# Kernel tuning notes

Hardware: AMD Instinct MI355X
Metric: run time of the kernel (lower is better)

## Reference

```python
import jax, jax.numpy as jnp
import numpy as np

N_NODES = 100000
N_EDGES = 625000
D_IN = 128
D_OUT = 128


def setup_inputs() -> dict:
    key = jax.random.key(0)
    k1, k2, k3, k4, k5 = jax.random.split(key, 5)
    scale = 1.0 / np.sqrt(D_IN)
    x = jax.random.normal(k1, (N_NODES, D_IN), dtype=jnp.float32)
    edge_index = jax.random.randint(k2, (2, N_EDGES), 0, N_NODES, dtype=jnp.int64)
    W_l = jax.random.normal(k3, (D_IN, D_OUT), dtype=jnp.float32) * scale
    b_l = jax.random.normal(k4, (D_OUT,), dtype=jnp.float32) * scale
    W_r = jax.random.normal(k5, (D_IN, D_OUT), dtype=jnp.float32) * scale
    return {"x": x, "edge_index": edge_index, "W_l": W_l, "b_l": b_l, "W_r": W_r}


def reference(x, edge_index, W_l, b_l, W_r):
    # SAGEConv (mean aggr, no self loops):
    #   out = lin_l(mean_{j in N(i)} x_j) + lin_r(x_i)
    src = edge_index[0]  # message source nodes
    dst = edge_index[1]  # aggregation targets
    n = x.shape[0]
    msgs = x[src]  # [E, D_IN] gather
    agg = jax.ops.segment_sum(msgs, dst, num_segments=n)  # [N, D_IN]
    deg = jax.ops.segment_sum(jnp.ones_like(dst, dtype=x.dtype), dst, num_segments=n)
    mean = agg / jnp.maximum(deg, 1.0)[:, None]  # isolated nodes -> 0
    return mean @ W_l + b_l + x @ W_r
```

## Files before the change

### kernel.cpp

```cpp
#include <hip/hip_runtime.h>


constexpr int N_NODES = 100000;
constexpr int N_EDGES = 625000;
constexpr int D = 128;
constexpr int SCAN_CHUNK = 1024;
constexpr int N_SCAN_BLOCKS = (N_NODES + SCAN_CHUNK - 1) / SCAN_CHUNK;
constexpr int CONV_BLOCKS = N_NODES * D / (512 * 4);
constexpr int ZERO_BLOCKS = (N_NODES / 4 + 255) / 256;
constexpr int E4 = N_EDGES / 4;

typedef __attribute__((ext_vector_type(8))) short short8;
typedef __attribute__((ext_vector_type(4))) short short4v;
typedef __attribute__((ext_vector_type(4))) float f32x4;

__device__ __forceinline__ unsigned short f2bf(float f) {
    union { float f; unsigned int u; } c; c.f = f;
    unsigned int u = c.u + 0x7fffu + ((c.u >> 16) & 1u);
    return (unsigned short)(u >> 16);
}
__device__ __forceinline__ float bflo(unsigned int v) {
    union { unsigned int u; float f; } c; c.u = v << 16; return c.f;
}
__device__ __forceinline__ float bfhi(unsigned int v) {
    union { unsigned int u; float f; } c; c.u = v & 0xffff0000u; return c.f;
}
__device__ __forceinline__ uint2 pack4(float4 a) {
    uint2 r;
    r.x = (unsigned)f2bf(a.x) | ((unsigned)f2bf(a.y) << 16);
    r.y = (unsigned)f2bf(a.z) | ((unsigned)f2bf(a.w) << 16);
    return r;
}

__global__ __launch_bounds__(256) void conv_all(
    const float* __restrict__ x, const float* __restrict__ Wl,
    const float* __restrict__ Wr,
    unsigned short* __restrict__ xb, unsigned short* __restrict__ wT,
    int* __restrict__ cnt)
{
    const int tid = threadIdx.x;
    if (blockIdx.x < CONV_BLOCKS) {
        __shared__ uint2 ls[512];
        const float4* xp = (const float4*)x;
        const int base = blockIdx.x * 512;
        float4 v0 = xp[base + tid];
        float4 v1 = xp[base + 256 + tid];
        ls[tid]       = pack4(v0);
        ls[tid + 256] = pack4(v1);
        __syncthreads();
        uint4 q = ((const uint4*)ls)[tid];
        ((uint4*)xb)[base / 2 + tid] = q;
    } else if (blockIdx.x < CONV_BLOCKS + 16) {
        int flat = (blockIdx.x - CONV_BLOCKS) * 256 + tid;
        int k  = flat >> 4;
        int n0 = (flat & 15) * 8;
        const float* Wsrc = (k < 128) ? &Wl[k * 128 + n0] : &Wr[(k - 128) * 128 + n0];
        float4 a = *(const float4*)Wsrc;
        float4 b = *(const float4*)(Wsrc + 4);
        wT[(n0 + 0) * 256 + k] = f2bf(a.x);
        wT[(n0 + 1) * 256 + k] = f2bf(a.y);
        wT[(n0 + 2) * 256 + k] = f2bf(a.z);
        wT[(n0 + 3) * 256 + k] = f2bf(a.w);
        wT[(n0 + 4) * 256 + k] = f2bf(b.x);
        wT[(n0 + 5) * 256 + k] = f2bf(b.y);
        wT[(n0 + 6) * 256 + k] = f2bf(b.z);
        wT[(n0 + 7) * 256 + k] = f2bf(b.w);
    } else {
        int t3 = (blockIdx.x - CONV_BLOCKS - 16) * 256 + tid;
        if (t3 < N_NODES / 4) ((uint4*)cnt)[t3] = make_uint4(0, 0, 0, 0);
    }
}

__global__ __launch_bounds__(256) void hist4(
    const int* __restrict__ dst, int* __restrict__ cnt)
{
    int t = blockIdx.x * 256 + threadIdx.x;
    if (t < E4) {
        int e = t * 4;
        int4 d4 = *(const int4*)&dst[e];
        atomicAdd(&cnt[d4.x], 1);
        atomicAdd(&cnt[d4.y], 1);
        atomicAdd(&cnt[d4.z], 1);
        atomicAdd(&cnt[d4.w], 1);
    }
}

__global__ __launch_bounds__(256) void scan_blocks(
    const int* __restrict__ cnt, int* __restrict__ ptr, int* __restrict__ bsums)
{
    __shared__ int sh[256];
    const int t = threadIdx.x;
    const int base = blockIdx.x * SCAN_CHUNK + t * 4;
    int v0 = (base + 0 < N_NODES) ? cnt[base + 0] : 0;
    int v1 = (base + 1 < N_NODES) ? cnt[base + 1] : 0;
    int v2 = (base + 2 < N_NODES) ? cnt[base + 2] : 0;
    int v3 = (base + 3 < N_NODES) ? cnt[base + 3] : 0;
    const int tsum = v0 + v1 + v2 + v3;
    sh[t] = tsum;
    __syncthreads();
    #pragma unroll
    for (int off = 1; off < 256; off <<= 1) {
        int val = (t >= off) ? sh[t - off] : 0;
        __syncthreads();
        sh[t] += val;
        __syncthreads();
    }
    const int texcl = sh[t] - tsum;
    if (t == 255) bsums[blockIdx.x] = sh[255];
    int e0 = texcl, e1 = e0 + v0, e2 = e1 + v1, e3 = e2 + v2;
    if (base + 0 < N_NODES) ptr[base + 0] = e0;
    if (base + 1 < N_NODES) ptr[base + 1] = e1;
    if (base + 2 < N_NODES) ptr[base + 2] = e2;
    if (base + 3 < N_NODES) ptr[base + 3] = e3;
}

__global__ __launch_bounds__(256) void add_offsets_fused(
    int* __restrict__ ptr, int* __restrict__ cursor, const int* __restrict__ bsums)
{
    __shared__ int sh[256];
    const int t = threadIdx.x;
    int v = (t < blockIdx.x) ? bsums[t] : 0;
    sh[t] = v;
    __syncthreads();
    #pragma unroll
    for (int off = 128; off > 0; off >>= 1) {
        if (t < off) sh[t] += sh[t + off];
        __syncthreads();
    }
    const int soff = sh[0];
    const int base = blockIdx.x * SCAN_CHUNK + t * 4;
    #pragma unroll
    for (int j = 0; j < 4; ++j) {
        int i = base + j;
        if (i < N_NODES) {
            int p = ptr[i] + soff;
            ptr[i] = p;
            cursor[i] = p;
        }
    }
    if (blockIdx.x == 0 && t == 0) ptr[N_NODES] = N_EDGES;
}

__global__ __launch_bounds__(256) void csr_fill(
    const int* __restrict__ src, const int* __restrict__ dst,
    int* __restrict__ cursor, int* __restrict__ sorted_src)
{
    int t = blockIdx.x * 256 + threadIdx.x;
    if (t < E4) {
        int e = t * 4;
        int4 d4 = *(const int4*)&dst[e];
        int4 s4 = *(const int4*)&src[e];
        int p0 = atomicAdd(&cursor[d4.x], 1);
        int p1 = atomicAdd(&cursor[d4.y], 1);
        int p2 = atomicAdd(&cursor[d4.z], 1);
        int p3 = atomicAdd(&cursor[d4.w], 1);
        sorted_src[p0] = s4.x;
        sorted_src[p1] = s4.y;
        sorted_src[p2] = s4.z;
        sorted_src[p3] = s4.w;
    }
}

__global__ __launch_bounds__(256) void sage_fused(
    const unsigned short* __restrict__ xb,
    const int* __restrict__ ptr,
    const int* __restrict__ sorted_src,
    const unsigned short* __restrict__ wT,
    const float* __restrict__ bl,
    float* __restrict__ out)
{
    __shared__ unsigned short sA[32 * 256];

    const int tid  = threadIdx.x;
    const int lane = tid & 63;
    const int w    = tid >> 6;
    const int l15  = lane & 15;
    const int lg   = lane >> 4;

    const int n0 = w * 32 + l15;
    const int n1 = n0 + 16;

    short8 B0[8], B1[8];
    #pragma unroll
    for (int s = 0; s < 8; ++s) {
        B0[s] = *(const short8*)&wT[(size_t)n0 * 256 + s * 32 + lg * 8];
        B1[s] = *(const short8*)&wT[(size_t)n1 * 256 + s * 32 + lg * 8];
    }
    const float bias0 = bl[n0];
    const float bias1 = bl[n1];

    const int row0 = blockIdx.x * 32;

    #pragma unroll
    for (int i = 0; i < 2; ++i) {
        int c = tid + i * 256;
        int r = c >> 4;
        int s = 16 + (c & 15);
        short8 v = *(const short8*)&xb[(size_t)(row0 + r) * D + (c & 15) * 8];
        *(short8*)&sA[r * 256 + ((s ^ (r & 7)) << 3)] = v;
    }

    {
        const int g = tid >> 4;
        const int l = tid & 15;
        const size_t off = (size_t)l * 8;

        auto gather_row = [&](int r) {
            const int node = row0 + r;
            const int beg = ptr[node];
            const int end = ptr[node + 1];
            float a0=0,a1=0,a2=0,a3=0,a4=0,a5=0,a6=0,a7=0;
            float b0=0,b1=0,b2=0,b3=0,b4=0,b5=0,b6=0,b7=0;
            float c0=0,c1=0,c2=0,c3=0,c4=0,c5=0,c6=0,c7=0;
            float d0=0,d1=0,d2=0,d3=0,d4=0,d5=0,d6=0,d7=0;
            for (int i = beg; i < end; i += 4) {
                int last = end - 1;
                int e1 = i + 1 < end ? i + 1 : last;
                int e2 = i + 2 < end ? i + 2 : last;
                int e3 = i + 3 < end ? i + 3 : last;
                float w1 = (i + 1 < end) ? 1.f : 0.f;
                float w2 = (i + 2 < end) ? 1.f : 0.f;
                float w3 = (i + 3 < end) ? 1.f : 0.f;
                int s0 = sorted_src[i],  s1 = sorted_src[e1];
                int s2 = sorted_src[e2], s3 = sorted_src[e3];
                uint4 v0 = *(const uint4*)&xb[(size_t)s0 * D + off];
                uint4 v1 = *(const uint4*)&xb[(size_t)s1 * D + off];
                uint4 v2 = *(const uint4*)&xb[(size_t)s2 * D + off];
                uint4 v3 = *(const uint4*)&xb[(size_t)s3 * D + off];
                a0+=bflo(v0.x); a1+=bfhi(v0.x); a2+=bflo(v0.y); a3+=bfhi(v0.y);
                a4+=bflo(v0.z); a5+=bfhi(v0.z); a6+=bflo(v0.w); a7+=bfhi(v0.w);
                b0=fmaf(w1,bflo(v1.x),b0); b1=fmaf(w1,bfhi(v1.x),b1);
                b2=fmaf(w1,bflo(v1.y),b2); b3=fmaf(w1,bfhi(v1.y),b3);
                b4=fmaf(w1,bflo(v1.z),b4); b5=fmaf(w1,bfhi(v1.z),b5);
                b6=fmaf(w1,bflo(v1.w),b6); b7=fmaf(w1,bfhi(v1.w),b7);
                c0=fmaf(w2,bflo(v2.x),c0); c1=fmaf(w2,bfhi(v2.x),c1);
                c2=fmaf(w2,bflo(v2.y),c2); c3=fmaf(w2,bfhi(v2.y),c3);
                c4=fmaf(w2,bflo(v2.z),c4); c5=fmaf(w2,bfhi(v2.z),c5);
                c6=fmaf(w2,bflo(v2.w),c6); c7=fmaf(w2,bfhi(v2.w),c7);
                d0=fmaf(w3,bflo(v3.x),d0); d1=fmaf(w3,bfhi(v3.x),d1);
                d2=fmaf(w3,bflo(v3.y),d2); d3=fmaf(w3,bfhi(v3.y),d3);
                d4=fmaf(w3,bflo(v3.z),d4); d5=fmaf(w3,bfhi(v3.z),d5);
                d6=fmaf(w3,bflo(v3.w),d6); d7=fmaf(w3,bfhi(v3.w),d7);
            }
            const float sc = 1.0f / fmaxf((float)(end - beg), 1.0f);
            uint4 o;
            o.x = (unsigned)f2bf(((a0+b0)+(c0+d0))*sc) | ((unsigned)f2bf(((a1+b1)+(c1+d1))*sc) << 16);
            o.y = (unsigned)f2bf(((a2+b2)+(c2+d2))*sc) | ((unsigned)f2bf(((a3+b3)+(c3+d3))*sc) << 16);
            o.z = (unsigned)f2bf(((a4+b4)+(c4+d4))*sc) | ((unsigned)f2bf(((a5+b5)+(c5+d5))*sc) << 16);
            o.w = (unsigned)f2bf(((a6+b6)+(c6+d6))*sc) | ((unsigned)f2bf(((a7+b7)+(c7+d7))*sc) << 16);
            *(uint4*)&sA[r * 256 + ((l ^ (r & 7)) << 3)] = o;
        };
        gather_row(g);
        gather_row(g + 16);
    }
    __syncthreads();

    const int a_r0 = l15;
    const int a_r1 = 16 + l15;

    f32x4 acc00 = {0.f,0.f,0.f,0.f}, acc01 = {0.f,0.f,0.f,0.f};
    f32x4 acc10 = {0.f,0.f,0.f,0.f}, acc11 = {0.f,0.f,0.f,0.f};

    #pragma unroll
    for (int s = 0; s < 8; ++s) {
        int ks = s * 4 + lg;
        short8 a0 = *(const short8*)&sA[a_r0 * 256 + ((ks ^ (a_r0 & 7)) << 3)];
        short8 a1 = *(const short8*)&sA[a_r1 * 256 + ((ks ^ (a_r1 & 7)) << 3)];
        acc00 = __builtin_amdgcn_mfma_f32_16x16x32_bf16(a0, B0[s], acc00, 0, 0, 0);
        acc01 = __builtin_amdgcn_mfma_f32_16x16x32_bf16(a0, B1[s], acc01, 0, 0, 0);
        acc10 = __builtin_amdgcn_mfma_f32_16x16x32_bf16(a1, B0[s], acc10, 0, 0, 0);
        acc11 = __builtin_amdgcn_mfma_f32_16x16x32_bf16(a1, B1[s], acc11, 0, 0, 0);
    }

    #pragma unroll
    for (int reg = 0; reg < 4; ++reg) {
        int r0w = row0 + lg * 4 + reg;
        int r1w = r0w + 16;
        out[(size_t)r0w * D + n0] = acc00[reg] + bias0;
        out[(size_t)r0w * D + n1] = acc01[reg] + bias1;
        out[(size_t)r1w * D + n0] = acc10[reg] + bias0;
        out[(size_t)r1w * D + n1] = acc11[reg] + bias1;
    }
}

__global__ __launch_bounds__(256) void wt_build(
    const float* __restrict__ Wl, const float* __restrict__ Wr,
    unsigned short* __restrict__ wT)
{
    int idx = blockIdx.x * 256 + threadIdx.x;
    if (idx >= 128 * 256) return;
    int n = idx >> 8;
    int k = idx & 255;
    float v = (k < 128) ? Wl[k * 128 + n] : Wr[(k - 128) * 128 + n];
    wT[n * 256 + k] = f2bf(v);
}

__global__ __launch_bounds__(256) void sage_aggregate(
    const float* __restrict__ x,
    const int* __restrict__ ptr,
    const int* __restrict__ sorted_src,
    float* __restrict__ mean)
{
    const int node = blockIdx.x * 4 + (threadIdx.x >> 6);
    if (node >= N_NODES) return;
    const int lane = threadIdx.x & 63;
    const int beg = ptr[node];
    const int end = ptr[node + 1];

    float2 acc0 = make_float2(0.f, 0.f);
    float2 acc1 = make_float2(0.f, 0.f);
    int i = beg;
    for (; i + 1 < end; i += 2) {
        int s0 = sorted_src[i];
        int s1 = sorted_src[i + 1];
        float2 a = *(const float2*)&x[(size_t)s0 * D + lane * 2];
        float2 b = *(const float2*)&x[(size_t)s1 * D + lane * 2];
        acc0.x += a.x; acc0.y += a.y;
        acc1.x += b.x; acc1.y += b.y;
    }
    if (i < end) {
        int s0 = sorted_src[i];
        float2 a = *(const float2*)&x[(size_t)s0 * D + lane * 2];
        acc0.x += a.x; acc0.y += a.y;
    }
    const float sc = 1.0f / fmaxf((float)(end - beg), 1.0f);
    float2 r = make_float2((acc0.x + acc1.x) * sc, (acc0.y + acc1.y) * sc);
    *(float2*)&mean[(size_t)node * D + lane * 2] = r;
}

__global__ __launch_bounds__(256) void sage_gemm_mfma(
    const float* __restrict__ x,
    const unsigned short* __restrict__ wT,
    const float* __restrict__ bl,
    float* __restrict__ out)
{
    __shared__ unsigned short sW[128 * 256];
    __shared__ unsigned short sA1[32 * 256];

    const int tid  = threadIdx.x;
    const int lane = tid & 63;
    const int w    = tid >> 6;
    const int l15  = lane & 15;
    const int lg   = lane >> 4;

    #pragma unroll
    for (int i = 0; i < 16; ++i) {
        int c  = tid + i * 256;
        int n  = c >> 5;
        int k8 = c & 31;
        short8 v = ((const short8*)wT)[c];
        *(short8*)&sW[n * 256 + ((k8 ^ (n & 7)) << 3)] = v;
    }

    const int a_r0 = l15;
    const int a_r1 = 16 + l15;
    const int n0 = w * 32 + l15;
    const int n1 = n0 + 16;
    const float bias0 = bl[n0];
    const float bias1 = bl[n1];
    const int nTiles = N_NODES / 32;

    for (int tile = blockIdx.x; tile < nTiles; tile += gridDim.x) {
        const int row0 = tile * 32;
        #pragma unroll
        for (int i = 0; i < 8; ++i) {
            int c    = tid + i * 256;
            int r    = c >> 6;
            int half = (c >> 5) & 1;
            int f4   = c & 31;
            const float* srcp = half ? &x[(size_t)(row0 + r) * D + f4 * 4]
                                     : &out[(size_t)(row0 + r) * D + f4 * 4];
            float4 v = *(const float4*)srcp;
            short4v b;
            b.x = (short)f2bf(v.x); b.y = (short)f2bf(v.y);
            b.z = (short)f2bf(v.z); b.w = (short)f2bf(v.w);
            int k = half * 128 + f4 * 4;
            int u = k >> 3;
            *(short4v*)&sA1[r * 256 + ((u ^ (r & 7)) << 3) + (k & 7)] = b;
        }
        __syncthreads();

        f32x4 acc00 = {0.f,0.f,0.f,0.f}, acc01 = {0.f,0.f,0.f,0.f};
        f32x4 acc10 = {0.f,0.f,0.f,0.f}, acc11 = {0.f,0.f,0.f,0.f};

        #pragma unroll
        for (int s = 0; s < 8; ++s) {
            int ks = s * 4 + lg;
            short8 a0 = *(const short8*)&sA1[a_r0 * 256 + ((ks ^ (a_r0 & 7)) << 3)];
            short8 a1 = *(const short8*)&sA1[a_r1 * 256 + ((ks ^ (a_r1 & 7)) << 3)];
            short8 b0 = *(const short8*)&sW[n0 * 256 + ((ks ^ (n0 & 7)) << 3)];
            short8 b1 = *(const short8*)&sW[n1 * 256 + ((ks ^ (n1 & 7)) << 3)];
            acc00 = __builtin_amdgcn_mfma_f32_16x16x32_bf16(a0, b0, acc00, 0, 0, 0);
            acc01 = __builtin_amdgcn_mfma_f32_16x16x32_bf16(a0, b1, acc01, 0, 0, 0);
            acc10 = __builtin_amdgcn_mfma_f32_16x16x32_bf16(a1, b0, acc10, 0, 0, 0);
            acc11 = __builtin_amdgcn_mfma_f32_16x16x32_bf16(a1, b1, acc11, 0, 0, 0);
        }
        __syncthreads();

        #pragma unroll
        for (int reg = 0; reg < 4; ++reg) {
            int r0w = row0 + lg * 4 + reg;
            int r1w = r0w + 16;
            out[(size_t)r0w * D + n0] = acc00[reg] + bias0;
            out[(size_t)r0w * D + n1] = acc01[reg] + bias1;
            out[(size_t)r1w * D + n0] = acc10[reg] + bias0;
            out[(size_t)r1w * D + n1] = acc11[reg] + bias1;
        }
    }
}

__global__ __launch_bounds__(256) void sage_scatter(
    const float* __restrict__ x, const int* __restrict__ src,
    const int* __restrict__ dst, float* __restrict__ agg, float* __restrict__ deg)
{
    int gid = blockIdx.x * 256 + threadIdx.x;
    int e = gid >> 7;
    if (e >= N_EDGES) return;
    int d = gid & 127;
    atomicAdd(&agg[(size_t)dst[e] * D + d], x[(size_t)src[e] * D + d]);
    if (d == 0) atomicAdd(&deg[dst[e]], 1.0f);
}

__global__ __launch_bounds__(256) void apply_mean(
    float* __restrict__ agg, const float* __restrict__ deg)
{
    int gid = blockIdx.x * 256 + threadIdx.x;
    int row = gid >> 5;
    if (row >= N_NODES) return;
    float sc = 1.0f / fmaxf(deg[row], 1.0f);
    float4 v = ((float4*)agg)[gid];
    v.x *= sc; v.y *= sc; v.z *= sc; v.w *= sc;
    ((float4*)agg)[gid] = v;
}

__device__ __forceinline__ void accum_tile(
    float acc[4][4], const float (*sWf)[D], const float (*srow)[D], int h, int j4)
{
    #pragma unroll 2
    for (int k = 0; k < D; k += 4) {
        float4 w0 = *(const float4*)&sWf[k + 0][j4];
        float4 w1 = *(const float4*)&sWf[k + 1][j4];
        float4 w2 = *(const float4*)&sWf[k + 2][j4];
        float4 w3 = *(const float4*)&sWf[k + 3][j4];
        #pragma unroll
        for (int r = 0; r < 4; ++r) {
            float4 a = *(const float4*)&srow[h + r * 8][k];
            acc[r][0] = fmaf(a.x, w0.x, fmaf(a.y, w1.x, fmaf(a.z, w2.x, fmaf(a.w, w3.x, acc[r][0]))));
            acc[r][1] = fmaf(a.x, w0.y, fmaf(a.y, w1.y, fmaf(a.z, w2.y, fmaf(a.w, w3.y, acc[r][1]))));
            acc[r][2] = fmaf(a.x, w0.z, fmaf(a.y, w1.z, fmaf(a.z, w2.z, fmaf(a.w, w3.z, acc[r][2]))));
            acc[r][3] = fmaf(a.x, w0.w, fmaf(a.y, w1.w, fmaf(a.z, w2.w, fmaf(a.w, w3.w, acc[r][3]))));
        }
    }
}

__global__ __launch_bounds__(256) void sage_gemm_f32(
    const float* __restrict__ x, const float* __restrict__ Wl,
    const float* __restrict__ bl, const float* __restrict__ Wr,
    float* __restrict__ out)
{
    __shared__ float sWf[D][D];
    __shared__ float srow[32][D];
    const int tid = threadIdx.x;
    const int j4 = (tid & 31) * 4;
    const int h  = tid >> 5;
    const int nTiles = (N_NODES + 31) / 32;
    const float4 bias = *(const float4*)(bl + j4);

    for (int tile = blockIdx.x; tile < nTiles; tile += gridDim.x) {
        const int row0 = tile * 32;
        float acc[4][4];
        #pragma unroll
        for (int r = 0; r < 4; ++r)
            #pragma unroll
            for (int c = 0; c < 4; ++c) acc[r][c] = 0.0f;

        __syncthreads();
        #pragma unroll
        for (int i = 0; i < 16; ++i)
            ((float4*)sWf)[tid + i * 256] = ((const float4*)Wl)[tid + i * 256];
        #pragma unroll
        for (int i = 0; i < 4; ++i) {
            int idx = tid + i * 256, r = idx >> 5, c = idx & 31, row = row0 + r;
            float4 v = make_float4(0.f,0.f,0.f,0.f);
            if (row < N_NODES) v = ((const float4*)out)[(size_t)row * 32 + c];
            ((float4*)srow)[idx] = v;
        }
        __syncthreads();
        accum_tile(acc, sWf, srow, h, j4);

        __syncthreads();
        #pragma unroll
        for (int i = 0; i < 16; ++i)
            ((float4*)sWf)[tid + i * 256] = ((const float4*)Wr)[tid + i * 256];
        #pragma unroll
        for (int i = 0; i < 4; ++i) {
            int idx = tid + i * 256, r = idx >> 5, c = idx & 31, row = row0 + r;
            float4 v = make_float4(0.f,0.f,0.f,0.f);
            if (row < N_NODES) v = ((const float4*)x)[(size_t)row * 32 + c];
            ((float4*)srow)[idx] = v;
        }
        __syncthreads();
        accum_tile(acc, sWf, srow, h, j4);

        #pragma unroll
        for (int r = 0; r < 4; ++r) {
            int row = row0 + h + r * 8;
            if (row < N_NODES) {
                float4 v = make_float4(acc[r][0] + bias.x, acc[r][1] + bias.y,
                                       acc[r][2] + bias.z, acc[r][3] + bias.w);
                *(float4*)(out + (size_t)row * D + j4) = v;
            }
        }
    }
}

extern "C" void kernel_launch(void* const* d_in, const int* in_sizes, int n_in,
                              void* d_out, int out_size, void* d_ws, size_t ws_size,
                              hipStream_t stream) {
    const float* x   = (const float*)d_in[0];
    const int*   ei  = (const int*)d_in[1];
    const float* Wl  = (const float*)d_in[2];
    const float* bl  = (const float*)d_in[3];
    const float* Wr  = (const float*)d_in[4];
    float* out = (float*)d_out;

    const int* src = ei;
    const int* dst = ei + N_EDGES;

    int* cnt    = (int*)d_ws;
    int* ptr    = cnt + N_NODES;
    int* cursor = ptr + N_NODES + 1;
    int* bsums  = cursor + N_NODES;
    int* sorted = bsums + 128;
    size_t int_count = (size_t)(3 * N_NODES + 1 + 128 + N_EDGES);
    int_count = (int_count + 7) & ~(size_t)7;
    unsigned short* wT = (unsigned short*)((int*)d_ws + int_count);
    unsigned short* xb = wT + 128 * 256;

    size_t need_B = int_count * sizeof(int);
    size_t need_A = need_B + 128 * 256 * 2 + (size_t)N_NODES * D * 2;

    if (ws_size >= need_A) {
        conv_all<<<CONV_BLOCKS + 16 + ZERO_BLOCKS, 256, 0, stream>>>(
            x, Wl, Wr, xb, wT, cnt);
        hist4<<<(E4 + 255) / 256, 256, 0, stream>>>(dst, cnt);
        scan_blocks<<<N_SCAN_BLOCKS, 256, 0, stream>>>(cnt, ptr, bsums);
        add_offsets_fused<<<N_SCAN_BLOCKS, 256, 0, stream>>>(ptr, cursor, bsums);
        csr_fill<<<(E4 + 255) / 256, 256, 0, stream>>>(src, dst, cursor, sorted);
        sage_fused<<<N_NODES / 32, 256, 0, stream>>>(xb, ptr, sorted, wT, bl, out);
    } else if (ws_size >= need_B) {
        hipMemsetAsync(cnt, 0, (size_t)N_NODES * sizeof(int), stream);
        hist4<<<(E4 + 255) / 256, 256, 0, stream>>>(dst, cnt);
        scan_blocks<<<N_SCAN_BLOCKS, 256, 0, stream>>>(cnt, ptr, bsums);
        add_offsets_fused<<<N_SCAN_BLOCKS, 256, 0, stream>>>(ptr, cursor, bsums);
        csr_fill<<<(E4 + 255) / 256, 256, 0, stream>>>(src, dst, cursor, sorted);
        unsigned short* wTc = (unsigned short*)cursor;
        wt_build<<<(128 * 256 + 255) / 256, 256, 0, stream>>>(Wl, Wr, wTc);
        sage_aggregate<<<(N_NODES + 3) / 4, 256, 0, stream>>>(x, ptr, sorted, out);
        sage_gemm_mfma<<<512, 256, 0, stream>>>(x, wTc, bl, out);
    } else {
        float* deg = (float*)d_ws;
        hipMemsetAsync(out, 0, (size_t)N_NODES * D * sizeof(float), stream);
        hipMemsetAsync(deg, 0, (size_t)N_NODES * sizeof(float), stream);
        long long total = (long long)N_EDGES * 128;
        sage_scatter<<<(int)((total + 255) / 256), 256, 0, stream>>>(x, src, dst, out, deg);
        apply_mean<<<(N_NODES * 32 + 255) / 256, 256, 0, stream>>>(out, deg);
        sage_gemm_f32<<<512, 256, 0, stream>>>(x, Wl, bl, Wr, out);
    }
}
```

Measured before the change: 139.5 us.

## Gather neighbor features from per-row int8-quantized copy instead of bf16

The conversion kernel now also writes an int8 copy of x with one absmax scale per row, alongside the bf16 copy. The fused SAGE kernel gathers neighbor rows from this int8 buffer, halving the bytes per random gather, and rescales each row by its scale during accumulation. Each thread now handles one node with 16 features instead of two nodes with 8, and the weight fragments load after the gather to lower register pressure during it. This adds quantization error to the mean aggregation, an extra write pass in the conversion kernel, and more dequantize ALU work.

```diff
diff --git a/kernel.cpp b/kernel.cpp
--- a/kernel.cpp
+++ b/kernel.cpp
@@ -6,7 +6,7 @@
 constexpr int D = 128;
 constexpr int SCAN_CHUNK = 1024;
 constexpr int N_SCAN_BLOCKS = (N_NODES + SCAN_CHUNK - 1) / SCAN_CHUNK;
-constexpr int CONV_BLOCKS = N_NODES * D / (512 * 4);
+constexpr int CONV2_BLOCKS = N_NODES / 16;
 constexpr int ZERO_BLOCKS = (N_NODES / 4 + 255) / 256;
 constexpr int E4 = N_EDGES / 4;
 
@@ -18,12 +18,6 @@
     union { float f; unsigned int u; } c; c.f = f;
     unsigned int u = c.u + 0x7fffu + ((c.u >> 16) & 1u);
     return (unsigned short)(u >> 16);
-}
-__device__ __forceinline__ float bflo(unsigned int v) {
-    union { unsigned int u; float f; } c; c.u = v << 16; return c.f;
-}
-__device__ __forceinline__ float bfhi(unsigned int v) {
-    union { unsigned int u; float f; } c; c.u = v & 0xffff0000u; return c.f;
 }
 __device__ __forceinline__ uint2 pack4(float4 a) {
     uint2 r;
@@ -31,27 +25,52 @@
     r.y = (unsigned)f2bf(a.z) | ((unsigned)f2bf(a.w) << 16);
     return r;
 }
+__device__ __forceinline__ void i8x4_to_f32(unsigned q, float* o) {
+    o[0] = (float)(int)(signed char)(q & 0xff);
+    o[1] = (float)(int)(signed char)((q >> 8) & 0xff);
+    o[2] = (float)(int)(signed char)((q >> 16) & 0xff);
+    o[3] = (float)(int)(signed char)(q >> 24);
+}
 
 __global__ __launch_bounds__(256) void conv_all(
     const float* __restrict__ x, const float* __restrict__ Wl,
     const float* __restrict__ Wr,
-    unsigned short* __restrict__ xb, unsigned short* __restrict__ wT,
-    int* __restrict__ cnt)
+    unsigned short* __restrict__ xb, unsigned char* __restrict__ x8,
+    float* __restrict__ scales,
+    unsigned short* __restrict__ wT, int* __restrict__ cnt)
 {
     const int tid = threadIdx.x;
-    if (blockIdx.x < CONV_BLOCKS) {
-        __shared__ uint2 ls[512];
+    if (blockIdx.x < CONV2_BLOCKS) {
+        const int g = tid >> 4;
+        const int l = tid & 15;
+        const int row = blockIdx.x * 16 + g;
         const float4* xp = (const float4*)x;
-        const int base = blockIdx.x * 512;
-        float4 v0 = xp[base + tid];
-        float4 v1 = xp[base + 256 + tid];
-        ls[tid]       = pack4(v0);
-        ls[tid + 256] = pack4(v1);
-        __syncthreads();
-        uint4 q = ((const uint4*)ls)[tid];
-        ((uint4*)xb)[base / 2 + tid] = q;
-    } else if (blockIdx.x < CONV_BLOCKS + 16) {
-        int flat = (blockIdx.x - CONV_BLOCKS) * 256 + tid;
+        const int f4a = row * 32 + l;
+        const int f4b = f4a + 16;
+        float4 v0 = xp[f4a];
+        float4 v1 = xp[f4b];
+        float m = fmaxf(fmaxf(fmaxf(fabsf(v0.x), fabsf(v0.y)), fmaxf(fabsf(v0.z), fabsf(v0.w))),
+                        fmaxf(fmaxf(fabsf(v1.x), fabsf(v1.y)), fmaxf(fabsf(v1.z), fabsf(v1.w))));
+        #pragma unroll
+        for (int off = 1; off < 16; off <<= 1)
+            m = fmaxf(m, __shfl_xor(m, off, 16));
+        const float s   = m * (1.0f / 127.0f);
+        const float inv = (m > 0.0f) ? 127.0f / m : 0.0f;
+        if (l == 0) scales[row] = s;
+        auto q4 = [&](float4 v) -> unsigned {
+            int a0 = (int)rintf(v.x * inv);
+            int a1 = (int)rintf(v.y * inv);
+            int a2 = (int)rintf(v.z * inv);
+            int a3 = (int)rintf(v.w * inv);
+            return (unsigned)(a0 & 0xff) | ((unsigned)(a1 & 0xff) << 8) |
+                   ((unsigned)(a2 & 0xff) << 16) | ((unsigned)(a3 & 0xff) << 24);
+        };
+        ((unsigned*)x8)[f4a] = q4(v0);
+        ((unsigned*)x8)[f4b] = q4(v1);
+        ((uint2*)xb)[f4a] = pack4(v0);
+        ((uint2*)xb)[f4b] = pack4(v1);
+    } else if (blockIdx.x < CONV2_BLOCKS + 16) {
+        int flat = (blockIdx.x - CONV2_BLOCKS) * 256 + tid;
         int k  = flat >> 4;
         int n0 = (flat & 15) * 8;
         const float* Wsrc = (k < 128) ? &Wl[k * 128 + n0] : &Wr[(k - 128) * 128 + n0];
@@ -66,7 +85,7 @@
         wT[(n0 + 6) * 256 + k] = f2bf(b.z);
         wT[(n0 + 7) * 256 + k] = f2bf(b.w);
     } else {
-        int t3 = (blockIdx.x - CONV_BLOCKS - 16) * 256 + tid;
+        int t3 = (blockIdx.x - CONV2_BLOCKS - 16) * 256 + tid;
         if (t3 < N_NODES / 4) ((uint4*)cnt)[t3] = make_uint4(0, 0, 0, 0);
     }
 }
@@ -163,6 +182,8 @@
 
 __global__ __launch_bounds__(256) void sage_fused(
     const unsigned short* __restrict__ xb,
+    const unsigned char* __restrict__ x8,
+    const float* __restrict__ scales,
     const int* __restrict__ ptr,
     const int* __restrict__ sorted_src,
     const unsigned short* __restrict__ wT,
@@ -176,18 +197,6 @@
     const int w    = tid >> 6;
     const int l15  = lane & 15;
     const int lg   = lane >> 4;
-
-    const int n0 = w * 32 + l15;
-    const int n1 = n0 + 16;
-
-    short8 B0[8], B1[8];
-    #pragma unroll
-    for (int s = 0; s < 8; ++s) {
-        B0[s] = *(const short8*)&wT[(size_t)n0 * 256 + s * 32 + lg * 8];
-        B1[s] = *(const short8*)&wT[(size_t)n1 * 256 + s * 32 + lg * 8];
-    }
-    const float bias0 = bl[n0];
-    const float bias1 = bl[n1];
 
     const int row0 = blockIdx.x * 32;
 
@@ -201,59 +210,92 @@
     }
 
     {
-        const int g = tid >> 4;
-        const int l = tid & 15;
-        const size_t off = (size_t)l * 8;
-
-        auto gather_row = [&](int r) {
-            const int node = row0 + r;
-            const int beg = ptr[node];
-            const int end = ptr[node + 1];
-            float a0=0,a1=0,a2=0,a3=0,a4=0,a5=0,a6=0,a7=0;
-            float b0=0,b1=0,b2=0,b3=0,b4=0,b5=0,b6=0,b7=0;
-            float c0=0,c1=0,c2=0,c3=0,c4=0,c5=0,c6=0,c7=0;
-            float d0=0,d1=0,d2=0,d3=0,d4=0,d5=0,d6=0,d7=0;
-            for (int i = beg; i < end; i += 4) {
-                int last = end - 1;
-                int e1 = i + 1 < end ? i + 1 : last;
-                int e2 = i + 2 < end ? i + 2 : last;
-                int e3 = i + 3 < end ? i + 3 : last;
-                float w1 = (i + 1 < end) ? 1.f : 0.f;
-                float w2 = (i + 2 < end) ? 1.f : 0.f;
-                float w3 = (i + 3 < end) ? 1.f : 0.f;
-                int s0 = sorted_src[i],  s1 = sorted_src[e1];
-                int s2 = sorted_src[e2], s3 = sorted_src[e3];
-                uint4 v0 = *(const uint4*)&xb[(size_t)s0 * D + off];
-                uint4 v1 = *(const uint4*)&xb[(size_t)s1 * D + off];
-                uint4 v2 = *(const uint4*)&xb[(size_t)s2 * D + off];
-                uint4 v3 = *(const uint4*)&xb[(size_t)s3 * D + off];
-                a0+=bflo(v0.x); a1+=bfhi(v0.x); a2+=bflo(v0.y); a3+=bfhi(v0.y);
-                a4+=bflo(v0.z); a5+=bfhi(v0.z); a6+=bflo(v0.w); a7+=bfhi(v0.w);
-                b0=fmaf(w1,bflo(v1.x),b0); b1=fmaf(w1,bfhi(v1.x),b1);
-                b2=fmaf(w1,bflo(v1.y),b2); b3=fmaf(w1,bfhi(v1.y),b3);
-                b4=fmaf(w1,bflo(v1.z),b4); b5=fmaf(w1,bfhi(v1.z),b5);
-                b6=fmaf(w1,bflo(v1.w),b6); b7=fmaf(w1,bfhi(v1.w),b7);
-                c0=fmaf(w2,bflo(v2.x),c0); c1=fmaf(w2,bfhi(v2.x),c1);
-                c2=fmaf(w2,bflo(v2.y),c2); c3=fmaf(w2,bfhi(v2.y),c3);
-                c4=fmaf(w2,bflo(v2.z),c4); c5=fmaf(w2,bfhi(v2.z),c5);
-                c6=fmaf(w2,bflo(v2.w),c6); c7=fmaf(w2,bfhi(v2.w),c7);
-                d0=fmaf(w3,bflo(v3.x),d0); d1=fmaf(w3,bfhi(v3.x),d1);
-                d2=fmaf(w3,bflo(v3.y),d2); d3=fmaf(w3,bfhi(v3.y),d3);
-                d4=fmaf(w3,bflo(v3.z),d4); d5=fmaf(w3,bfhi(v3.z),d5);
-                d6=fmaf(w3,bflo(v3.w),d6); d7=fmaf(w3,bfhi(v3.w),d7);
-            }
-            const float sc = 1.0f / fmaxf((float)(end - beg), 1.0f);
-            uint4 o;
-            o.x = (unsigned)f2bf(((a0+b0)+(c0+d0))*sc) | ((unsigned)f2bf(((a1+b1)+(c1+d1))*sc) << 16);
-            o.y = (unsigned)f2bf(((a2+b2)+(c2+d2))*sc) | ((unsigned)f2bf(((a3+b3)+(c3+d3))*sc) << 16);
-            o.z = (unsigned)f2bf(((a4+b4)+(c4+d4))*sc) | ((unsigned)f2bf(((a5+b5)+(c5+d5))*sc) << 16);
-            o.w = (unsigned)f2bf(((a6+b6)+(c6+d6))*sc) | ((unsigned)f2bf(((a7+b7)+(c7+d7))*sc) << 16);
-            *(uint4*)&sA[r * 256 + ((l ^ (r & 7)) << 3)] = o;
-        };
-        gather_row(g);
-        gather_row(g + 16);
+        const int g = tid >> 3;
+        const int l = tid & 7;
+        const size_t off8 = (size_t)l * 16;
+        const int node = row0 + g;
+        const int beg = ptr[node];
+        const int end = ptr[node + 1];
+
+        float acc[4][16];
+        #pragma unroll
+        for (int a = 0; a < 4; ++a)
+            #pragma unroll
+            for (int j = 0; j < 16; ++j) acc[a][j] = 0.0f;
+
+        for (int i = beg; i < end; i += 4) {
+            int last = end - 1;
+            int e1 = i + 1 < end ? i + 1 : last;
+            int e2 = i + 2 < end ? i + 2 : last;
+            int e3 = i + 3 < end ? i + 3 : last;
+            float w1 = (i + 1 < end) ? 1.f : 0.f;
+            float w2 = (i + 2 < end) ? 1.f : 0.f;
+            float w3 = (i + 3 < end) ? 1.f : 0.f;
+            int s0 = sorted_src[i],  s1 = sorted_src[e1];
+            int s2 = sorted_src[e2], s3 = sorted_src[e3];
+            uint4 q0 = *(const uint4*)&x8[(size_t)s0 * D + off8];
+            uint4 q1 = *(const uint4*)&x8[(size_t)s1 * D + off8];
+            uint4 q2 = *(const uint4*)&x8[(size_t)s2 * D + off8];
+            uint4 q3 = *(const uint4*)&x8[(size_t)s3 * D + off8];
+            float ws0 = scales[s0];
+            float ws1 = w1 * scales[s1];
+            float ws2 = w2 * scales[s2];
+            float ws3 = w3 * scales[s3];
+
+            float t[16];
+            i8x4_to_f32(q0.x, &t[0]);  i8x4_to_f32(q0.y, &t[4]);
+            i8x4_to_f32(q0.z, &t[8]);  i8x4_to_f32(q0.w, &t[12]);
+            #pragma unroll
+            for (int j = 0; j < 16; ++j) acc[0][j] = fmaf(ws0, t[j], acc[0][j]);
+
+            i8x4_to_f32(q1.x, &t[0]);  i8x4_to_f32(q1.y, &t[4]);
+            i8x4_to_f32(q1.z, &t[8]);  i8x4_to_f32(q1.w, &t[12]);
+            #pragma unroll
+            for (int j = 0; j < 16; ++j) acc[1][j] = fmaf(ws1, t[j], acc[1][j]);
+
+            i8x4_to_f32(q2.x, &t[0]);  i8x4_to_f32(q2.y, &t[4]);
+            i8x4_to_f32(q2.z, &t[8]);  i8x4_to_f32(q2.w, &t[12]);
+            #pragma unroll
+            for (int j = 0; j < 16; ++j) acc[2][j] = fmaf(ws2, t[j], acc[2][j]);
+
+            i8x4_to_f32(q3.x, &t[0]);  i8x4_to_f32(q3.y, &t[4]);
+            i8x4_to_f32(q3.z, &t[8]);  i8x4_to_f32(q3.w, &t[12]);
+            #pragma unroll
+            for (int j = 0; j < 16; ++j) acc[3][j] = fmaf(ws3, t[j], acc[3][j]);
+        }
+
+        const float sc = 1.0f / fmaxf((float)(end - beg), 1.0f);
+        float m[16];
+        #pragma unroll
+        for (int j = 0; j < 16; ++j)
+            m[j] = ((acc[0][j] + acc[1][j]) + (acc[2][j] + acc[3][j])) * sc;
+
+        uint4 o_lo, o_hi;
+        o_lo.x = (unsigned)f2bf(m[0])  | ((unsigned)f2bf(m[1])  << 16);
+        o_lo.y = (unsigned)f2bf(m[2])  | ((unsigned)f2bf(m[3])  << 16);
+        o_lo.z = (unsigned)f2bf(m[4])  | ((unsigned)f2bf(m[5])  << 16);
+        o_lo.w = (unsigned)f2bf(m[6])  | ((unsigned)f2bf(m[7])  << 16);
+        o_hi.x = (unsigned)f2bf(m[8])  | ((unsigned)f2bf(m[9])  << 16);
+        o_hi.y = (unsigned)f2bf(m[10]) | ((unsigned)f2bf(m[11]) << 16);
+        o_hi.z = (unsigned)f2bf(m[12]) | ((unsigned)f2bf(m[13]) << 16);
+        o_hi.w = (unsigned)f2bf(m[14]) | ((unsigned)f2bf(m[15]) << 16);
+        int s0s = 2 * l;
+        int s1s = 2 * l + 1;
+        *(uint4*)&sA[g * 256 + ((s0s ^ (g & 7)) << 3)] = o_lo;
+        *(uint4*)&sA[g * 256 + ((s1s ^ (g & 7)) << 3)] = o_hi;
     }
     __syncthreads();
+
+    const int n0 = w * 32 + l15;
+    const int n1 = n0 + 16;
+    short8 B0[8], B1[8];
+    #pragma unroll
+    for (int s = 0; s < 8; ++s) {
+        B0[s] = *(const short8*)&wT[(size_t)n0 * 256 + s * 32 + lg * 8];
+        B1[s] = *(const short8*)&wT[(size_t)n1 * 256 + s * 32 + lg * 8];
+    }
+    const float bias0 = bl[n0];
+    const float bias1 = bl[n1];
 
     const int a_r0 = l15;
     const int a_r1 = 16 + l15;
@@ -536,18 +578,22 @@
     int_count = (int_count + 7) & ~(size_t)7;
     unsigned short* wT = (unsigned short*)((int*)d_ws + int_count);
     unsigned short* xb = wT + 128 * 256;
+    unsigned char*  x8 = (unsigned char*)(xb + (size_t)N_NODES * D);
+    float* scales      = (float*)(x8 + (size_t)N_NODES * D);
 
     size_t need_B = int_count * sizeof(int);
-    size_t need_A = need_B + 128 * 256 * 2 + (size_t)N_NODES * D * 2;
+    size_t need_A = need_B + 128 * 256 * 2 + (size_t)N_NODES * D * 2
+                    + (size_t)N_NODES * D + (size_t)N_NODES * 4;
 
     if (ws_size >= need_A) {
-        conv_all<<<CONV_BLOCKS + 16 + ZERO_BLOCKS, 256, 0, stream>>>(
-            x, Wl, Wr, xb, wT, cnt);
+        conv_all<<<CONV2_BLOCKS + 16 + ZERO_BLOCKS, 256, 0, stream>>>(
+            x, Wl, Wr, xb, x8, scales, wT, cnt);
         hist4<<<(E4 + 255) / 256, 256, 0, stream>>>(dst, cnt);
         scan_blocks<<<N_SCAN_BLOCKS, 256, 0, stream>>>(cnt, ptr, bsums);
         add_offsets_fused<<<N_SCAN_BLOCKS, 256, 0, stream>>>(ptr, cursor, bsums);
         csr_fill<<<(E4 + 255) / 256, 256, 0, stream>>>(src, dst, cursor, sorted);
-        sage_fused<<<N_NODES / 32, 256, 0, stream>>>(xb, ptr, sorted, wT, bl, out);
+        sage_fused<<<N_NODES / 32, 256, 0, stream>>>(
+            xb, x8, scales, ptr, sorted, wT, bl, out);
     } else if (ws_size >= need_B) {
         hipMemsetAsync(cnt, 0, (size_t)N_NODES * sizeof(int), stream);
         hist4<<<(E4 + 255) / 256, 256, 0, stream>>>(dst, cnt);
```

After: 133.8 us (median of 2 runs). 1.04x faster.
